# Optimization experiments

Measured on AMD Instinct MI355X. Metric: run time of the kernel, lower is better.

The kernel has to match this reference:

```python
import jax, jax.numpy as jnp
import numpy as np

B, S, D = 2, 1024, 768
NH = 12
DH = D // NH
HID = 1536
G, EPG = 4, 2
E = G * EPG
TEMP = 1.0
LN_EPS = 1e-5


def setup_inputs() -> dict:
    key = jax.random.key(0)
    ks = jax.random.split(key, 8)
    s = 0.02
    return {
        "x": jax.random.normal(ks[0], (B, S, D), jnp.float32),
        "ln1_w": jnp.ones((D,), jnp.float32),
        "ln1_b": jnp.zeros((D,), jnp.float32),
        "in_proj_w": jax.random.normal(ks[1], (3 * D, D), jnp.float32) * s,
        "in_proj_b": jnp.zeros((3 * D,), jnp.float32),
        "out_proj_w": jax.random.normal(ks[2], (D, D), jnp.float32) * s,
        "out_proj_b": jnp.zeros((D,), jnp.float32),
        "ln2_w": jnp.ones((D,), jnp.float32),
        "ln2_b": jnp.zeros((D,), jnp.float32),
        "Wg": jax.random.normal(ks[3], (D, G), jnp.float32) * s,
        "bg": jnp.zeros((G,), jnp.float32),
        "We": jax.random.normal(ks[4], (G, D, EPG), jnp.float32) * s,
        "be": jnp.zeros((G, EPG), jnp.float32),
        "W1": jax.random.normal(ks[5], (E, D, HID), jnp.float32) * s,
        "b1": jnp.zeros((E, HID), jnp.float32),
        "W2": jax.random.normal(ks[6], (E, HID, D), jnp.float32) * s,
        "b2": jnp.zeros((E, D), jnp.float32),
    }


def _ln(x, w, b):
    m = x.mean(-1, keepdims=True)
    v = x.var(-1, keepdims=True)
    return (x - m) / jnp.sqrt(v + LN_EPS) * w + b


def _mha(h, wqkv, bqkv, wo, bo):
    qkv = h @ wqkv.T + bqkv                       # [B,S,3D]
    q, k, v = jnp.split(qkv, 3, axis=-1)
    q = q.reshape(B, S, NH, DH)
    k = k.reshape(B, S, NH, DH)
    v = v.reshape(B, S, NH, DH)
    scale = 1.0 / np.sqrt(DH).astype(np.float32)
    att = jnp.einsum("bqhd,bkhd->bhqk", q, k) * scale
    p = jax.nn.softmax(att, axis=-1)
    o = jnp.einsum("bhqk,bkhd->bqhd", p, v).reshape(B, S, D)
    return o @ wo.T + bo


def _moe(h, Wg, bg, We, be, W1, b1, W2, b2):
    hf = h.reshape(-1, D)                         # [N,D] tokens
    # level-1: group router (temperature softmax, top-1)
    gp = jax.nn.softmax((hf @ Wg + bg) / TEMP, axis=-1)          # [N,G]
    g = jnp.argmax(gp, axis=-1)                                   # [N]
    pg = jnp.take_along_axis(gp, g[:, None], axis=1)[:, 0]        # [N]
    # level-2: within-group expert router
    el = jnp.einsum("nd,gde->nge", hf, We) + be                   # [N,G,EPG]
    ep = jax.nn.softmax(el / TEMP, axis=-1)
    ep_g = jnp.take_along_axis(ep, g[:, None, None], axis=1)[:, 0, :]  # [N,EPG]
    e = jnp.argmax(ep_g, axis=-1)                                 # [N]
    pe = jnp.take_along_axis(ep_g, e[:, None], axis=1)[:, 0]      # [N]
    flat = g * EPG + e                                            # flat expert id [N]
    combine = jax.nn.one_hot(flat, E, dtype=hf.dtype) * (pg * pe)[:, None]  # [N,E]
    # dense expert compute (reference form of dispatch/grouped-GEMM/combine)
    hid = jax.nn.gelu(jnp.einsum("nd,edh->enh", hf, W1) + b1[:, None, :])   # [E,N,HID]
    y = jnp.einsum("enh,ehd->end", hid, W2) + b2[:, None, :]                # [E,N,D]
    out = jnp.einsum("ne,end->nd", combine, y)                              # [N,D]
    return out.reshape(h.shape)


def reference(x, ln1_w, ln1_b, in_proj_w, in_proj_b, out_proj_w, out_proj_b,
              ln2_w, ln2_b, Wg, bg, We, be, W1, b1, W2, b2):
    a = _mha(_ln(x, ln1_w, ln1_b), in_proj_w, in_proj_b, out_proj_w, out_proj_b)
    x = x + a  # dropout p=0.0 -> identity
    m = _moe(_ln(x, ln2_w, ln2_b), Wg, bg, We, be, W1, b1, W2, b2)
    return x + m
```

## Files before the change

### kernel.cpp

```cpp
#include <hip/hip_runtime.h>
#include <stdint.h>

#define B_ 2
#define S_ 1024
#define D_ 768
#define NH_ 12
#define DH_ 64
#define HID_ 1536
#define G_ 4
#define EPG_ 2
#define E_ 8
#define NTOK (B_*S_)
#define NGRP (B_*NH_*16)
#define KSPLIT 3

typedef unsigned short u16;
typedef unsigned int u32;
typedef __bf16 bf16x8 __attribute__((ext_vector_type(8)));
typedef float f32x4 __attribute__((ext_vector_type(4)));
typedef u16 u16x4 __attribute__((ext_vector_type(4)));
typedef u16 u16x8 __attribute__((ext_vector_type(8)));
typedef u32 u32x4 __attribute__((ext_vector_type(4)));

struct BfPair { u16 hi, lo; };

__device__ __forceinline__ u16 f2bf(float f){
  unsigned u = __builtin_bit_cast(unsigned, f);
  u += 0x7FFFu + ((u >> 16) & 1u);
  return (u16)(u >> 16);
}
__device__ __forceinline__ float bf2f(u16 h){
  unsigned u = ((unsigned)h) << 16;
  return __builtin_bit_cast(float, u);
}
__device__ __forceinline__ BfPair split_bf(float v){
  BfPair p;
  p.hi = f2bf(v);
  p.lo = f2bf(v - bf2f(p.hi));
  return p;
}
__device__ __forceinline__ float gelu_tanh(float x){
  float t = 0.7978845608028654f * (x + 0.044715f * x * x * x);
  float e = __expf(2.f * t);
  float th = 1.f - 2.f / (e + 1.f);
  return 0.5f * x * (1.f + th);
}
__device__ __forceinline__ void gload_lds16(const void* g, void* l){
  __builtin_amdgcn_global_load_lds(
      (const __attribute__((address_space(1))) void*)g,
      (__attribute__((address_space(3))) void*)l, 16, 0, 0);
}

__global__ __launch_bounds__(256) void k_prep(
    const float* __restrict__ in_proj_w, const float* __restrict__ out_proj_w,
    const float* __restrict__ W1, const float* __restrict__ W2,
    u16* __restrict__ inpTh, u16* __restrict__ inpTl,
    u16* __restrict__ outpTh, u16* __restrict__ outpTl,
    u16* __restrict__ W1t, u16* __restrict__ W2t){
  __shared__ float tile[32][33];
  int bid = blockIdx.x, t = threadIdx.x;
  if (bid < 2304){
    const float* src; u16 *dh, *dl; int i;
    if (bid < 1728){ src = in_proj_w; dh = inpTh; dl = inpTl; i = bid * 256 + t; }
    else           { src = out_proj_w; dh = outpTh; dl = outpTl; i = (bid - 1728) * 256 + t; }
    float4 v = ((const float4*)src)[i];
    u16x4 oh, ol;
    BfPair p0 = split_bf(v.x), p1 = split_bf(v.y), p2 = split_bf(v.z), p3 = split_bf(v.w);
    oh.x = p0.hi; ol.x = p0.lo; oh.y = p1.hi; ol.y = p1.lo;
    oh.z = p2.hi; ol.z = p2.lo; oh.w = p3.hi; ol.w = p3.lo;
    ((u16x4*)dh)[i] = oh;
    ((u16x4*)dl)[i] = ol;
  } else {
    const float* src; u16* dst; int R, C, cx, cy, e;
    if (bid < 11520){
      int r = bid - 2304; e = r / 1152; r %= 1152;
      R = D_; C = HID_; cx = r % 48; cy = r / 48;
      src = W1; dst = W1t;
    } else {
      int r = bid - 11520; e = r / 1152; r %= 1152;
      R = HID_; C = D_; cx = r % 24; cy = r / 24;
      src = W2; dst = W2t;
    }
    const float* s = src + (size_t)e * R * C;
    u16* d = dst + (size_t)e * R * C;
    int c0 = cx * 32, r0 = cy * 32;
    int tx = t & 31, ty = t >> 5;
    #pragma unroll
    for (int i = 0; i < 32; i += 8)
      tile[ty + i][tx] = s[(size_t)(r0 + ty + i) * C + c0 + tx];
    __syncthreads();
    #pragma unroll
    for (int i = 0; i < 32; i += 8)
      d[(size_t)(c0 + ty + i) * R + r0 + tx] = f2bf(tile[tx][ty + i]);
  }
}

__global__ __launch_bounds__(256) void k_layernorm(
    const float* __restrict__ x, const float* __restrict__ w, const float* __restrict__ b,
    u16* __restrict__ oh, u16* __restrict__ ol, float* __restrict__ of){
  int row = blockIdx.x;
  const float* xr = x + (size_t)row * D_;
  int t = threadIdx.x;
  float v0 = xr[t], v1 = xr[t + 256], v2 = xr[t + 512];
  float s = v0 + v1 + v2;
  float sq = v0 * v0 + v1 * v1 + v2 * v2;
  #pragma unroll
  for (int m = 1; m < 64; m <<= 1){ s += __shfl_xor(s, m); sq += __shfl_xor(sq, m); }
  __shared__ float ls[4], lq[4];
  int wid = t >> 6;
  if ((t & 63) == 0){ ls[wid] = s; lq[wid] = sq; }
  __syncthreads();
  s = ls[0] + ls[1] + ls[2] + ls[3];
  sq = lq[0] + lq[1] + lq[2] + lq[3];
  float mean = s * (1.f / D_);
  float var = sq * (1.f / D_) - mean * mean;
  float rstd = rsqrtf(var + 1e-5f);
  #pragma unroll
  for (int i = 0; i < 3; i++){
    int dcol = t + i * 256;
    float v = (i == 0 ? v0 : (i == 1 ? v1 : v2));
    float y = (v - mean) * rstd * w[dcol] + b[dcol];
    BfPair p = split_bf(y);
    oh[(size_t)row * D_ + dcol] = p.hi;
    if (ol) ol[(size_t)row * D_ + dcol] = p.lo;
    if (of) of[(size_t)row * D_ + dcol] = y;
  }
}

template<int EPI>
__global__ __launch_bounds__(256) void k_gemm3(
    const u16* __restrict__ Ah, const u16* __restrict__ Al,
    const u16* __restrict__ Bh, const u16* __restrict__ Bl,
    const float* __restrict__ bias, const float* __restrict__ resid,
    u16* __restrict__ outh, u16* __restrict__ outl, float* __restrict__ outf,
    u16* __restrict__ vth, u16* __restrict__ vtl,
    int M, int N, int K){
  __shared__ alignas(16) u16 Ash[2][128 * 32];
  __shared__ alignas(16) u16 Asl[2][128 * 32];
  __shared__ alignas(16) u16 Bsh[2][64 * 32];
  __shared__ alignas(16) u16 Bsl[2][64 * 32];
  int m0 = blockIdx.x * 128, n0 = blockIdx.y * 64;
  int tid = threadIdx.x, w = tid >> 6, l = tid & 63;
  f32x4 acc[2][4];
  #pragma unroll
  for (int i = 0; i < 2; i++)
    #pragma unroll
    for (int j = 0; j < 4; j++) acc[i][j] = f32x4{0.f, 0.f, 0.f, 0.f};
  int srow = l >> 2;
  int scol = 8 * ((l & 3) ^ ((l >> 2) & 3));
  const u16* gAh0 = Ah + (size_t)(m0 + w * 32 + srow) * K + scol;
  const u16* gAh1 = gAh0 + (size_t)16 * K;
  const u16* gAl0 = Al + (size_t)(m0 + w * 32 + srow) * K + scol;
  const u16* gAl1 = gAl0 + (size_t)16 * K;
  const u16* gBh = Bh + (size_t)(n0 + w * 16 + srow) * K + scol;
  const u16* gBl = Bl + (size_t)(n0 + w * 16 + srow) * K + scol;
  int dA0 = (w * 32) * 32, dA1 = (w * 32 + 16) * 32, dB = (w * 16) * 32;
  auto STAGE = [&](int buf, int k0){
    gload_lds16(gAh0 + k0, &Ash[buf][dA0]);
    gload_lds16(gAh1 + k0, &Ash[buf][dA1]);
    gload_lds16(gAl0 + k0, &Asl[buf][dA0]);
    gload_lds16(gAl1 + k0, &Asl[buf][dA1]);
    gload_lds16(gBh + k0, &Bsh[buf][dB]);
    gload_lds16(gBl + k0, &Bsl[buf][dB]);
  };
  STAGE(0, 0);
  __syncthreads();
  int nk = K / 32;
  int ca = (l >> 4) ^ (l & 3);
  int ai0 = (w * 32 + (l & 15)) * 32 + 8 * ca;
  int ai1 = ai0 + 16 * 32;
  for (int t = 0; t < nk; t++){
    int cur = t & 1;
    if (t + 1 < nk) STAGE(cur ^ 1, (t + 1) * 32);
    bf16x8 afh[2], afl[2], bfh[4], bfl[4];
    afh[0] = *(const bf16x8*)&Ash[cur][ai0];
    afh[1] = *(const bf16x8*)&Ash[cur][ai1];
    afl[0] = *(const bf16x8*)&Asl[cur][ai0];
    afl[1] = *(const bf16x8*)&Asl[cur][ai1];
    #pragma unroll
    for (int ni = 0; ni < 4; ni++){
      int bi = (ni * 16 + (l & 15)) * 32 + 8 * ca;
      bfh[ni] = *(const bf16x8*)&Bsh[cur][bi];
      bfl[ni] = *(const bf16x8*)&Bsl[cur][bi];
    }
    #pragma unroll
    for (int mi = 0; mi < 2; mi++)
      #pragma unroll
      for (int ni = 0; ni < 4; ni++){
        acc[mi][ni] = __builtin_amdgcn_mfma_f32_16x16x32_bf16(afh[mi], bfh[ni], acc[mi][ni], 0, 0, 0);
        acc[mi][ni] = __builtin_amdgcn_mfma_f32_16x16x32_bf16(afh[mi], bfl[ni], acc[mi][ni], 0, 0, 0);
        acc[mi][ni] = __builtin_amdgcn_mfma_f32_16x16x32_bf16(afl[mi], bfh[ni], acc[mi][ni], 0, 0, 0);
      }
    __syncthreads();
  }
  int r4 = (l >> 4) * 4, cc = l & 15;
  if (EPI == 0 && n0 >= 2 * D_){
    int hh = (n0 - 2 * D_) >> 6;
    int bb = m0 / S_;
    int bhl = bb * NH_ + hh;
    int sg0 = m0 % S_;
    u16* VhL = (u16*)&Ash[0][0];
    u16* VlL = (u16*)&Asl[0][0];
    #pragma unroll
    for (int mi = 0; mi < 2; mi++){
      #pragma unroll
      for (int ni = 0; ni < 4; ni++){
        int d = ni * 16 + cc;
        float bv = bias ? bias[n0 + d] : 0.f;
        int sl = w * 32 + mi * 16 + r4;
        u16x4 h4, l4;
        #pragma unroll
        for (int r = 0; r < 4; r++){
          BfPair p = split_bf(acc[mi][ni][r] + bv);
          h4[r] = p.hi; l4[r] = p.lo;
        }
        *(u16x4*)&VhL[d * 128 + sl] = h4;
        *(u16x4*)&VlL[d * 128 + sl] = l4;
      }
    }
    __syncthreads();
    for (int i = tid; i < 64 * 16; i += 256){
      int d = i >> 4, s8 = (i & 15) * 8;
      size_t go = ((size_t)bhl * DH_ + d) * S_ + sg0 + s8;
      *(u16x8*)&vth[go] = *(const u16x8*)&VhL[d * 128 + s8];
      *(u16x8*)&vtl[go] = *(const u16x8*)&VlL[d * 128 + s8];
    }
    return;
  }
  #pragma unroll
  for (int mi = 0; mi < 2; mi++){
    #pragma unroll
    for (int ni = 0; ni < 4; ni++){
      int col = n0 + ni * 16 + cc;
      float bv = bias ? bias[col] : 0.f;
      #pragma unroll
      for (int r = 0; r < 4; r++){
        int row = m0 + w * 32 + mi * 16 + r4 + r;
        float v = acc[mi][ni][r] + bv;
        if (EPI == 0){
          BfPair p = split_bf(v);
          outh[(size_t)row * N + col] = p.hi;
          outl[(size_t)row * N + col] = p.lo;
        } else {
          outf[(size_t)row * N + col] = v + resid[(size_t)row * N + col];
        }
      }
    }
  }
}

__global__ __launch_bounds__(256) void k_attn3(
    const u16* __restrict__ qkvh, const u16* __restrict__ qkvl,
    const u16* __restrict__ vth, const u16* __restrict__ vtl,
    float* __restrict__ po0, float* __restrict__ po1, float* __restrict__ po2,
    float* __restrict__ pm, float* __restrict__ plsum){
  __shared__ alignas(16) u16 Ksh[2][32 * 64];
  __shared__ alignas(16) u16 Ksl[2][32 * 64];
  __shared__ alignas(16) u16 Vsh[2][64 * 32];
  __shared__ alignas(16) u16 Vsl[2][64 * 32];
  int bh = blockIdx.x, qb = blockIdx.y, ks = blockIdx.z;
  int b = bh / NH_, h = bh % NH_;
  int g = bh * 16 + qb;
  int tid = threadIdx.x, w = tid >> 6, l = tid & 63;
  int q0 = qb * 64 + w * 16;
  const int RS = 3 * D_;
  size_t qoff = (size_t)(b * S_ + q0 + (l & 15)) * RS + h * DH_ + 8 * (l >> 4);
  bf16x8 aqh[2], aql[2];
  aqh[0] = *(const bf16x8*)(qkvh + qoff); aqh[1] = *(const bf16x8*)(qkvh + qoff + 32);
  aql[0] = *(const bf16x8*)(qkvl + qoff); aql[1] = *(const bf16x8*)(qkvl + qoff + 32);
  f32x4 oacc[4];
  #pragma unroll
  for (int i = 0; i < 4; i++) oacc[i] = f32x4{0.f, 0.f, 0.f, 0.f};
  float mrun = -1e30f, lrun = 0.f;

  size_t koff = (size_t)(b * S_ + w * 8 + (l >> 3)) * RS + D_ + h * DH_ + 8 * ((l & 7) ^ (l >> 3));
  const u16* Kgh = qkvh + koff;
  const u16* Kgl = qkvl + koff;
  size_t voff = ((size_t)bh * DH_ + w * 16 + (l >> 2)) * S_ + 8 * ((l & 3) ^ ((l >> 2) & 3));
  const u16* Vgh = vth + voff;
  const u16* Vgl = vtl + voff;
  int wdst = w * 512;

  auto STAGE = [&](int buf, int akt){
    gload_lds16(Kgh + (size_t)(akt * 32) * RS, &Ksh[buf][wdst]);
    gload_lds16(Kgl + (size_t)(akt * 32) * RS, &Ksl[buf][wdst]);
    gload_lds16(Vgh + akt * 32, &Vsh[buf][wdst]);
    gload_lds16(Vgl + akt * 32, &Vsl[buf][wdst]);
  };
  int kt0 = (ks * 32) / KSPLIT;
  int ktE = ((ks + 1) * 32) / KSPLIT;
  STAGE(0, kt0);
  __syncthreads();

  int ck0 = (l >> 4) ^ (l & 7);
  int ck1 = ck0 ^ 4;
  int cv = (l >> 4) ^ (l & 3);
  int s1 = (l & 15) | ((l & 16) << 1);
  int s2 = s1 + 16;
  bool up = (l & 32) != 0;

  for (int kt = kt0; kt < ktE; kt++){
    int cur = (kt - kt0) & 1;
    if (kt + 1 < ktE) STAGE(cur ^ 1, kt + 1);
    f32x4 st[2];
    #pragma unroll
    for (int nt = 0; nt < 2; nt++){
      int rbase = (nt * 16 + (l & 15)) * 64;
      bf16x8 kh0 = *(const bf16x8*)&Ksh[cur][rbase + 8 * ck0];
      bf16x8 kh1 = *(const bf16x8*)&Ksh[cur][rbase + 8 * ck1];
      bf16x8 kl0 = *(const bf16x8*)&Ksl[cur][rbase + 8 * ck0];
      bf16x8 kl1 = *(const bf16x8*)&Ksl[cur][rbase + 8 * ck1];
      f32x4 c = f32x4{0.f, 0.f, 0.f, 0.f};
      c = __builtin_amdgcn_mfma_f32_16x16x32_bf16(kh0, aqh[0], c, 0, 0, 0);
      c = __builtin_amdgcn_mfma_f32_16x16x32_bf16(kh1, aqh[1], c, 0, 0, 0);
      c = __builtin_amdgcn_mfma_f32_16x16x32_bf16(kh0, aql[0], c, 0, 0, 0);
      c = __builtin_amdgcn_mfma_f32_16x16x32_bf16(kh1, aql[1], c, 0, 0, 0);
      c = __builtin_amdgcn_mfma_f32_16x16x32_bf16(kl0, aqh[0], c, 0, 0, 0);
      c = __builtin_amdgcn_mfma_f32_16x16x32_bf16(kl1, aqh[1], c, 0, 0, 0);
      st[nt] = c;
    }
    float mx = fmaxf(fmaxf(fmaxf(st[0][0], st[0][1]), fmaxf(st[0][2], st[0][3])),
                     fmaxf(fmaxf(st[1][0], st[1][1]), fmaxf(st[1][2], st[1][3])));
    mx = fmaxf(mx, __shfl_xor(mx, 16));
    mx = fmaxf(mx, __shfl_xor(mx, 32));
    mx *= 0.125f;
    if (!__all(mx <= mrun)){
      float mnew = fmaxf(mrun, mx);
      float alpha = __expf(mrun - mnew);
      lrun *= alpha;
      #pragma unroll
      for (int r = 0; r < 4; r++){
        float ar = __shfl(alpha, (l & 48) | (((l >> 4) << 2) + r));
        oacc[0][r] *= ar; oacc[1][r] *= ar; oacc[2][r] *= ar; oacc[3][r] *= ar;
      }
      mrun = mnew;
    }
    float p[8]; float sum = 0.f;
    #pragma unroll
    for (int j = 0; j < 8; j++){
      p[j] = __expf(st[j >> 2][j & 3] * 0.125f - mrun);
      sum += p[j];
    }
    sum += __shfl_xor(sum, 16);
    sum += __shfl_xor(sum, 32);
    lrun += sum;
    u32 pkh[4], pkl[4];
    #pragma unroll
    for (int i = 0; i < 4; i++){
      BfPair a = split_bf(p[2 * i]), bb = split_bf(p[2 * i + 1]);
      pkh[i] = (u32)a.hi | ((u32)bb.hi << 16);
      pkl[i] = (u32)a.lo | ((u32)bb.lo << 16);
    }
    u32 ah0 = __shfl((int)pkh[0], s1), ah1 = __shfl((int)pkh[1], s1);
    u32 ah2 = __shfl((int)pkh[2], s1), ah3 = __shfl((int)pkh[3], s1);
    u32 bh0 = __shfl((int)pkh[0], s2), bh1 = __shfl((int)pkh[1], s2);
    u32 bh2 = __shfl((int)pkh[2], s2), bh3 = __shfl((int)pkh[3], s2);
    u32 al0 = __shfl((int)pkl[0], s1), al1 = __shfl((int)pkl[1], s1);
    u32 al2 = __shfl((int)pkl[2], s1), al3 = __shfl((int)pkl[3], s1);
    u32 bl0 = __shfl((int)pkl[0], s2), bl1 = __shfl((int)pkl[1], s2);
    u32 bl2 = __shfl((int)pkl[2], s2), bl3 = __shfl((int)pkl[3], s2);
    u32x4 fh, fl;
    fh.x = up ? ah2 : ah0; fh.y = up ? ah3 : ah1; fh.z = up ? bh2 : bh0; fh.w = up ? bh3 : bh1;
    fl.x = up ? al2 : al0; fl.y = up ? al3 : al1; fl.z = up ? bl2 : bl0; fl.w = up ? bl3 : bl1;
    bf16x8 pa_h = __builtin_bit_cast(bf16x8, fh);
    bf16x8 pa_l = __builtin_bit_cast(bf16x8, fl);
    #pragma unroll
    for (int dt = 0; dt < 4; dt++){
      int vb = (dt * 16 + (l & 15)) * 32 + 8 * cv;
      bf16x8 bvh = *(const bf16x8*)&Vsh[cur][vb];
      bf16x8 bvl = *(const bf16x8*)&Vsl[cur][vb];
      oacc[dt] = __builtin_amdgcn_mfma_f32_16x16x32_bf16(pa_h, bvh, oacc[dt], 0, 0, 0);
      oacc[dt] = __builtin_amdgcn_mfma_f32_16x16x32_bf16(pa_h, bvl, oacc[dt], 0, 0, 0);
      oacc[dt] = __builtin_amdgcn_mfma_f32_16x16x32_bf16(pa_l, bvh, oacc[dt], 0, 0, 0);
    }
    __syncthreads();
  }
  float* po = (ks == 0) ? po0 : ((ks == 1) ? po1 : po2);
  #pragma unroll
  for (int dt = 0; dt < 4; dt++)
    #pragma unroll
    for (int r = 0; r < 4; r++){
      int qloc = w * 16 + (l >> 4) * 4 + r;
      int d = dt * 16 + (l & 15);
      po[((size_t)(g * 64 + qloc)) * 64 + d] = oacc[dt][r];
    }
  if (l < 16){
    pm[(ks * NGRP + g) * 64 + w * 16 + l] = mrun;
    plsum[(ks * NGRP + g) * 64 + w * 16 + l] = lrun;
  }
}

__global__ __launch_bounds__(256) void k_attn_merge(
    const float* __restrict__ po0, const float* __restrict__ po1, const float* __restrict__ po2,
    const float* __restrict__ pm, const float* __restrict__ plsum,
    u16* __restrict__ oh, u16* __restrict__ ol){
  int bh = blockIdx.x, qb = blockIdx.y;
  int b = bh / NH_, h = bh % NH_;
  int g = bh * 16 + qb;
  int t = threadIdx.x;
  int q = t >> 2, d0 = (t & 3) * 16;
  float m0 = pm[g * 64 + q];
  float m1 = pm[(NGRP + g) * 64 + q];
  float m2 = pm[(2 * NGRP + g) * 64 + q];
  float l0 = plsum[g * 64 + q];
  float l1 = plsum[(NGRP + g) * 64 + q];
  float l2 = plsum[(2 * NGRP + g) * 64 + q];
  float M = fmaxf(fmaxf(m0, m1), m2);
  float a0 = __expf(m0 - M), a1 = __expf(m1 - M), a2 = __expf(m2 - M);
  float rcp = 1.f / (l0 * a0 + l1 * a1 + l2 * a2);
  size_t base = ((size_t)(g * 64 + q)) * 64 + d0;
  size_t orow = (size_t)(b * S_ + qb * 64 + q) * D_ + h * DH_ + d0;
  #pragma unroll
  for (int j = 0; j < 16; j++){
    float v = (po0[base + j] * a0 + po1[base + j] * a1 + po2[base + j] * a2) * rcp;
    BfPair p = split_bf(v);
    oh[orow + j] = p.hi;
    ol[orow + j] = p.lo;
  }
}

__global__ __launch_bounds__(256) void k_router(
    const float* __restrict__ h2f, const float* __restrict__ Wg, const float* __restrict__ bg,
    const float* __restrict__ We, const float* __restrict__ be,
    int* __restrict__ flat, float* __restrict__ pc){
  int w = threadIdx.x >> 6, l = threadIdx.x & 63;
  int n = blockIdx.x * 4 + w;
  const float* hr = h2f + (size_t)n * D_;
  float pl[4] = {0.f, 0.f, 0.f, 0.f};
  for (int d = l; d < D_; d += 64){
    float hv = hr[d];
    float4 wg = *(const float4*)&Wg[d * 4];
    pl[0] += hv * wg.x; pl[1] += hv * wg.y; pl[2] += hv * wg.z; pl[3] += hv * wg.w;
  }
  #pragma unroll
  for (int m = 1; m < 64; m <<= 1)
    #pragma unroll
    for (int g = 0; g < 4; g++) pl[g] += __shfl_xor(pl[g], m);
  float lg[4];
  #pragma unroll
  for (int g = 0; g < 4; g++) lg[g] = pl[g] + bg[g];
  int gi = 0; float gm = lg[0];
  #pragma unroll
  for (int g = 1; g < 4; g++) if (lg[g] > gm){ gm = lg[g]; gi = g; }
  float gs = 0.f;
  #pragma unroll
  for (int g = 0; g < 4; g++) gs += expf(lg[g] - gm);
  float pg = 1.f / gs;
  float e0 = 0.f, e1 = 0.f;
  for (int d = l; d < D_; d += 64){
    float hv = hr[d];
    float2 we = *(const float2*)&We[((size_t)gi * D_ + d) * 2];
    e0 += hv * we.x; e1 += hv * we.y;
  }
  #pragma unroll
  for (int m = 1; m < 64; m <<= 1){ e0 += __shfl_xor(e0, m); e1 += __shfl_xor(e1, m); }
  e0 += be[gi * 2]; e1 += be[gi * 2 + 1];
  int ei; float pe;
  if (e1 > e0){ ei = 1; pe = 1.f / (1.f + expf(e0 - e1)); }
  else        { ei = 0; pe = 1.f / (1.f + expf(e1 - e0)); }
  if (l == 0){
    flat[n] = gi * 2 + ei;
    pc[n] = pg * pe;
  }
}

__global__ __launch_bounds__(1024) void k_bucket(
    const int* __restrict__ flat, int* __restrict__ moeI, int* __restrict__ order){
  __shared__ int cnt[E_], off[E_], cur[E_];
  int t = threadIdx.x;
  if (t < E_){ cnt[t] = 0; cur[t] = 0; }
  __syncthreads();
  int n0 = t, n1 = t + 1024;
  int f0 = flat[n0], f1 = flat[n1];
  atomicAdd(&cnt[f0], 1);
  atomicAdd(&cnt[f1], 1);
  __syncthreads();
  if (t == 0){
    int s = 0;
    for (int e = 0; e < E_; e++){
      off[e] = s; moeI[16 + e] = s; moeI[e] = cnt[e]; s += cnt[e];
    }
  }
  __syncthreads();
  int p0 = atomicAdd(&cur[f0], 1);
  order[off[f0] + p0] = n0;
  int p1 = atomicAdd(&cur[f1], 1);
  order[off[f1] + p1] = n1;
}

__global__ __launch_bounds__(256) void k_moe_gemm1(
    const u16* __restrict__ h2, const u16* __restrict__ W1t, const float* __restrict__ b1,
    const int* __restrict__ order, const int* __restrict__ moeI, u16* __restrict__ hid){
  int e = blockIdx.x, mt = blockIdx.y, nt = blockIdx.z;
  int cnt = moeI[e];
  if (mt * 64 >= cnt) return;
  int off = moeI[16 + e];
  __shared__ alignas(16) u16 As[2][64 * 64];
  __shared__ alignas(16) u16 Bs[2][64 * 64];
  int tid = threadIdx.x, w = tid >> 6, l = tid & 63;
  int wr = w >> 1, wc = w & 1;
  f32x4 acc[2][2];
  #pragma unroll
  for (int i = 0; i < 2; i++)
    #pragma unroll
    for (int j = 0; j < 2; j++) acc[i][j] = f32x4{0.f, 0.f, 0.f, 0.f};
  int r0 = w * 16 + (l >> 3);
  int sch = 8 * ((l & 7) ^ (l >> 3));
  int tokA0 = order[off + min(mt * 64 + r0, cnt - 1)];
  int tokA1 = order[off + min(mt * 64 + r0 + 8, cnt - 1)];
  const u16* gA0 = h2 + (size_t)tokA0 * D_ + sch;
  const u16* gA1 = h2 + (size_t)tokA1 * D_ + sch;
  const u16* gB0 = W1t + (size_t)e * HID_ * D_ + (size_t)(nt * 64 + r0) * D_ + sch;
  const u16* gB1 = gB0 + (size_t)8 * D_;
  int d0 = (w * 16) * 64, d1 = (w * 16 + 8) * 64;
  auto STAGE = [&](int buf, int k0){
    gload_lds16(gA0 + k0, &As[buf][d0]);
    gload_lds16(gA1 + k0, &As[buf][d1]);
    gload_lds16(gB0 + k0, &Bs[buf][d0]);
    gload_lds16(gB1 + k0, &Bs[buf][d1]);
  };
  STAGE(0, 0);
  __syncthreads();
  int c0 = (l >> 4) ^ (l & 7);
  int c1 = ((l >> 4) + 4) ^ (l & 7);
  const int nk = D_ / 64;
  for (int t = 0; t < nk; t++){
    int cur = t & 1;
    if (t + 1 < nk) STAGE(cur ^ 1, (t + 1) * 64);
    bf16x8 af[2][2], bfr[2][2];
    #pragma unroll
    for (int mi = 0; mi < 2; mi++){
      int rbase = (wr * 32 + mi * 16 + (l & 15)) * 64;
      af[mi][0] = *(const bf16x8*)&As[cur][rbase + 8 * c0];
      af[mi][1] = *(const bf16x8*)&As[cur][rbase + 8 * c1];
    }
    #pragma unroll
    for (int ni = 0; ni < 2; ni++){
      int rbase = (wc * 32 + ni * 16 + (l & 15)) * 64;
      bfr[ni][0] = *(const bf16x8*)&Bs[cur][rbase + 8 * c0];
      bfr[ni][1] = *(const bf16x8*)&Bs[cur][rbase + 8 * c1];
    }
    #pragma unroll
    for (int mi = 0; mi < 2; mi++)
      #pragma unroll
      for (int ni = 0; ni < 2; ni++){
        acc[mi][ni] = __builtin_amdgcn_mfma_f32_16x16x32_bf16(af[mi][0], bfr[ni][0], acc[mi][ni], 0, 0, 0);
        acc[mi][ni] = __builtin_amdgcn_mfma_f32_16x16x32_bf16(af[mi][1], bfr[ni][1], acc[mi][ni], 0, 0, 0);
      }
    __syncthreads();
  }
  int r4 = (l >> 4) * 4, cc = l & 15;
  #pragma unroll
  for (int mi = 0; mi < 2; mi++){
    #pragma unroll
    for (int ni = 0; ni < 2; ni++){
      int col = nt * 64 + wc * 32 + ni * 16 + cc;
      float bv = b1[e * HID_ + col];
      #pragma unroll
      for (int r = 0; r < 4; r++){
        int rowl = mt * 64 + wr * 32 + mi * 16 + r4 + r;
        if (rowl < cnt){
          float v = gelu_tanh(acc[mi][ni][r] + bv);
          hid[(size_t)(off + rowl) * HID_ + col] = f2bf(v);
        }
      }
    }
  }
}

__global__ __launch_bounds__(256) void k_moe_gemm2(
    const u16* __restrict__ hid, const u16* __restrict__ W2t, const float* __restrict__ b2,
    const int* __restrict__ order, const int* __restrict__ moeI,
    const float* __restrict__ pc, const float* __restrict__ x2, float* __restrict__ out){
  int e = blockIdx.x, mt = blockIdx.y, nt = blockIdx.z;
  int cnt = moeI[e];
  if (mt * 64 >= cnt) return;
  int off = moeI[16 + e];
  __shared__ alignas(16) u16 As[2][64 * 64];
  __shared__ alignas(16) u16 Bs[2][64 * 64];
  int tid = threadIdx.x, w = tid >> 6, l = tid & 63;
  int wr = w >> 1, wc = w & 1;
  f32x4 acc[2][2];
  #pragma unroll
  for (int i = 0; i < 2; i++)
    #pragma unroll
    for (int j = 0; j < 2; j++) acc[i][j] = f32x4{0.f, 0.f, 0.f, 0.f};
  int r0 = w * 16 + (l >> 3);
  int sch = 8 * ((l & 7) ^ (l >> 3));
  int ar0 = off + min(mt * 64 + r0, cnt - 1);
  int ar1 = off + min(mt * 64 + r0 + 8, cnt - 1);
  const u16* gA0 = hid + (size_t)ar0 * HID_ + sch;
  const u16* gA1 = hid + (size_t)ar1 * HID_ + sch;
  const u16* gB0 = W2t + (size_t)e * D_ * HID_ + (size_t)(nt * 64 + r0) * HID_ + sch;
  const u16* gB1 = gB0 + (size_t)8 * HID_;
  int d0 = (w * 16) * 64, d1 = (w * 16 + 8) * 64;
  auto STAGE = [&](int buf, int k0){
    gload_lds16(gA0 + k0, &As[buf][d0]);
    gload_lds16(gA1 + k0, &As[buf][d1]);
    gload_lds16(gB0 + k0, &Bs[buf][d0]);
    gload_lds16(gB1 + k0, &Bs[buf][d1]);
  };
  STAGE(0, 0);
  __syncthreads();
  int c0 = (l >> 4) ^ (l & 7);
  int c1 = ((l >> 4) + 4) ^ (l & 7);
  const int nk = HID_ / 64;
  for (int t = 0; t < nk; t++){
    int cur = t & 1;
    if (t + 1 < nk) STAGE(cur ^ 1, (t + 1) * 64);
    bf16x8 af[2][2], bfr[2][2];
    #pragma unroll
    for (int mi = 0; mi < 2; mi++){
      int rbase = (wr * 32 + mi * 16 + (l & 15)) * 64;
      af[mi][0] = *(const bf16x8*)&As[cur][rbase + 8 * c0];
      af[mi][1] = *(const bf16x8*)&As[cur][rbase + 8 * c1];
    }
    #pragma unroll
    for (int ni = 0; ni < 2; ni++){
      int rbase = (wc * 32 + ni * 16 + (l & 15)) * 64;
      bfr[ni][0] = *(const bf16x8*)&Bs[cur][rbase + 8 * c0];
      bfr[ni][1] = *(const bf16x8*)&Bs[cur][rbase + 8 * c1];
    }
    #pragma unroll
    for (int mi = 0; mi < 2; mi++)
      #pragma unroll
      for (int ni = 0; ni < 2; ni++){
        acc[mi][ni] = __builtin_amdgcn_mfma_f32_16x16x32_bf16(af[mi][0], bfr[ni][0], acc[mi][ni], 0, 0, 0);
        acc[mi][ni] = __builtin_amdgcn_mfma_f32_16x16x32_bf16(af[mi][1], bfr[ni][1], acc[mi][ni], 0, 0, 0);
      }
    __syncthreads();
  }
  int r4 = (l >> 4) * 4, cc = l & 15;
  #pragma unroll
  for (int mi = 0; mi < 2; mi++){
    #pragma unroll
    for (int r = 0; r < 4; r++){
      int rowl = mt * 64 + wr * 32 + mi * 16 + r4 + r;
      if (rowl < cnt){
        int tok = order[off + rowl];
        float pv = pc[tok];
        #pragma unroll
        for (int ni = 0; ni < 2; ni++){
          int col = nt * 64 + wc * 32 + ni * 16 + cc;
          float v = acc[mi][ni][r] + b2[e * D_ + col];
          out[(size_t)tok * D_ + col] = x2[(size_t)tok * D_ + col] + pv * v;
        }
      }
    }
  }
}

extern "C" void kernel_launch(void* const* d_in, const int* in_sizes, int n_in,
                              void* d_out, int out_size, void* d_ws, size_t ws_size,
                              hipStream_t stream){
  const float* x         = (const float*)d_in[0];
  const float* ln1_w     = (const float*)d_in[1];
  const float* ln1_b     = (const float*)d_in[2];
  const float* in_proj_w = (const float*)d_in[3];
  const float* in_proj_b = (const float*)d_in[4];
  const float* out_proj_w= (const float*)d_in[5];
  const float* out_proj_b= (const float*)d_in[6];
  const float* ln2_w     = (const float*)d_in[7];
  const float* ln2_b     = (const float*)d_in[8];
  const float* Wg        = (const float*)d_in[9];
  const float* bg        = (const float*)d_in[10];
  const float* We        = (const float*)d_in[11];
  const float* be        = (const float*)d_in[12];
  const float* W1        = (const float*)d_in[13];
  const float* b1        = (const float*)d_in[14];
  const float* W2        = (const float*)d_in[15];
  const float* b2        = (const float*)d_in[16];
  float* out = (float*)d_out;

  char* ws = (char*)d_ws;
  size_t off = 0;
  auto alloc = [&](size_t bytes) -> char* {
    char* p = ws + off;
    off += (bytes + 255) & ~(size_t)255;
    return p;
  };
  u16*   inpTh = (u16*)  alloc((size_t)3 * D_ * D_ * 2);
  u16*   inpTl = (u16*)  alloc((size_t)3 * D_ * D_ * 2);
  u16*   outpTh= (u16*)  alloc((size_t)D_ * D_ * 2);
  u16*   outpTl= (u16*)  alloc((size_t)D_ * D_ * 2);
  u16*   W1t  = (u16*)  alloc((size_t)E_ * HID_ * D_ * 2);
  u16*   W2t  = (u16*)  alloc((size_t)E_ * D_ * HID_ * 2);
  u16*   qkvh = (u16*)  alloc((size_t)NTOK * 3 * D_ * 2);
  u16*   qkvl = (u16*)  alloc((size_t)NTOK * 3 * D_ * 2);
  u16*   h1h  = (u16*)  alloc((size_t)NTOK * D_ * 2);
  u16*   h1l  = (u16*)  alloc((size_t)NTOK * D_ * 2);
  u16*   vth  = (u16*)  alloc((size_t)B_ * NH_ * DH_ * S_ * 2);
  u16*   vtl  = (u16*)  alloc((size_t)B_ * NH_ * DH_ * S_ * 2);
  float* x2   = (float*)alloc((size_t)NTOK * D_ * 4);
  u16*   h2   = (u16*)  alloc((size_t)NTOK * D_ * 2);
  int*   flat = (int*)  alloc(NTOK * 4);
  float* pc   = (float*)alloc(NTOK * 4);
  int*   order= (int*)  alloc(NTOK * 4);
  int*   moeI = (int*)  alloc(32 * 4);
  float* po0  = (float*)h1h;
  float* po1  = (float*)inpTh;
  float* po2  = x2;
  float* pmArr= (float*)((char*)inpTh + 6291456);
  float* plArr= (float*)((char*)inpTh + 6291456 + 294912);
  u16*   attnh= qkvh;
  u16*   attnl= qkvl;
  float* h2f  = (float*)qkvh;
  u16*   hid  = (u16*)qkvl;

  k_prep<<<dim3(20736), dim3(256), 0, stream>>>(
      in_proj_w, out_proj_w, W1, W2, inpTh, inpTl, outpTh, outpTl, W1t, W2t);
  k_layernorm<<<dim3(NTOK), dim3(256), 0, stream>>>(x, ln1_w, ln1_b, h1h, h1l, (float*)nullptr);
  k_gemm3<0><<<dim3(NTOK / 128, 3 * D_ / 64), dim3(256), 0, stream>>>(
      h1h, h1l, inpTh, inpTl, in_proj_b, nullptr, qkvh, qkvl, nullptr, vth, vtl, NTOK, 3 * D_, D_);
  k_attn3<<<dim3(B_ * NH_, S_ / 64, KSPLIT), dim3(256), 0, stream>>>(
      qkvh, qkvl, vth, vtl, po0, po1, po2, pmArr, plArr);
  k_attn_merge<<<dim3(B_ * NH_, S_ / 64), dim3(256), 0, stream>>>(
      po0, po1, po2, pmArr, plArr, attnh, attnl);
  k_gemm3<1><<<dim3(NTOK / 128, D_ / 64), dim3(256), 0, stream>>>(
      attnh, attnl, outpTh, outpTl, out_proj_b, x, nullptr, nullptr, x2,
      (u16*)nullptr, (u16*)nullptr, NTOK, D_, D_);
  k_layernorm<<<dim3(NTOK), dim3(256), 0, stream>>>(x2, ln2_w, ln2_b, h2, (u16*)nullptr, h2f);
  k_router<<<dim3(NTOK / 4), dim3(256), 0, stream>>>(h2f, Wg, bg, We, be, flat, pc);
  k_bucket<<<dim3(1), dim3(1024), 0, stream>>>(flat, moeI, order);
  k_moe_gemm1<<<dim3(E_, NTOK / 64, HID_ / 64), dim3(256), 0, stream>>>(h2, W1t, b1, order, moeI, hid);
  k_moe_gemm2<<<dim3(E_, NTOK / 64, D_ / 64), dim3(256), 0, stream>>>(hid, W2t, b2, order, moeI, pc, x2, out);
}
```

Before: 207.7 us.

## Process two 16-row query tiles per wave in split-K attention

Each wave of the attention kernel now handles 32 query rows (two 16-row groups) instead of 16, so each workgroup covers 128 queries and the grid's query dimension halves. Every K/V tile staged into LDS is reused across twice as many queries, which halves the global-to-LDS traffic and the barrier count per query. In exchange, each thread holds more registers (two sets of accumulators, Q fragments and softmax state), which may lower occupancy. The grid also shrinks to 24x8x3 blocks, which may leave compute units underused. Output indexing is rewritten so the merge kernel's layout stays the same.

```diff
diff --git a/kernel.cpp b/kernel.cpp
--- a/kernel.cpp
+++ b/kernel.cpp
@@ -260,18 +260,21 @@
   __shared__ alignas(16) u16 Vsl[2][64 * 32];
   int bh = blockIdx.x, qb = blockIdx.y, ks = blockIdx.z;
   int b = bh / NH_, h = bh % NH_;
-  int g = bh * 16 + qb;
   int tid = threadIdx.x, w = tid >> 6, l = tid & 63;
-  int q0 = qb * 64 + w * 16;
   const int RS = 3 * D_;
-  size_t qoff = (size_t)(b * S_ + q0 + (l & 15)) * RS + h * DH_ + 8 * (l >> 4);
-  bf16x8 aqh[2], aql[2];
-  aqh[0] = *(const bf16x8*)(qkvh + qoff); aqh[1] = *(const bf16x8*)(qkvh + qoff + 32);
-  aql[0] = *(const bf16x8*)(qkvl + qoff); aql[1] = *(const bf16x8*)(qkvl + qoff + 32);
-  f32x4 oacc[4];
-  #pragma unroll
-  for (int i = 0; i < 4; i++) oacc[i] = f32x4{0.f, 0.f, 0.f, 0.f};
-  float mrun = -1e30f, lrun = 0.f;
+  bf16x8 aqh[2][2], aql[2][2];
+  #pragma unroll
+  for (int G = 0; G < 2; G++){
+    size_t qoff = (size_t)(b * S_ + qb * 128 + w * 32 + G * 16 + (l & 15)) * RS + h * DH_ + 8 * (l >> 4);
+    aqh[G][0] = *(const bf16x8*)(qkvh + qoff); aqh[G][1] = *(const bf16x8*)(qkvh + qoff + 32);
+    aql[G][0] = *(const bf16x8*)(qkvl + qoff); aql[G][1] = *(const bf16x8*)(qkvl + qoff + 32);
+  }
+  f32x4 oacc[2][4];
+  #pragma unroll
+  for (int G = 0; G < 2; G++)
+    #pragma unroll
+    for (int i = 0; i < 4; i++) oacc[G][i] = f32x4{0.f, 0.f, 0.f, 0.f};
+  float mrun[2] = {-1e30f, -1e30f}, lrun[2] = {0.f, 0.f};
 
   size_t koff = (size_t)(b * S_ + w * 8 + (l >> 3)) * RS + D_ + h * DH_ + 8 * ((l & 7) ^ (l >> 3));
   const u16* Kgh = qkvh + koff;
@@ -302,7 +305,7 @@
   for (int kt = kt0; kt < ktE; kt++){
     int cur = (kt - kt0) & 1;
     if (kt + 1 < ktE) STAGE(cur ^ 1, kt + 1);
-    f32x4 st[2];
+    f32x4 st[2][2];
     #pragma unroll
     for (int nt = 0; nt < 2; nt++){
       int rbase = (nt * 16 + (l & 15)) * 64;
@@ -310,83 +313,99 @@
       bf16x8 kh1 = *(const bf16x8*)&Ksh[cur][rbase + 8 * ck1];
       bf16x8 kl0 = *(const bf16x8*)&Ksl[cur][rbase + 8 * ck0];
       bf16x8 kl1 = *(const bf16x8*)&Ksl[cur][rbase + 8 * ck1];
-      f32x4 c = f32x4{0.f, 0.f, 0.f, 0.f};
-      c = __builtin_amdgcn_mfma_f32_16x16x32_bf16(kh0, aqh[0], c, 0, 0, 0);
-      c = __builtin_amdgcn_mfma_f32_16x16x32_bf16(kh1, aqh[1], c, 0, 0, 0);
-      c = __builtin_amdgcn_mfma_f32_16x16x32_bf16(kh0, aql[0], c, 0, 0, 0);
-      c = __builtin_amdgcn_mfma_f32_16x16x32_bf16(kh1, aql[1], c, 0, 0, 0);
-      c = __builtin_amdgcn_mfma_f32_16x16x32_bf16(kl0, aqh[0], c, 0, 0, 0);
-      c = __builtin_amdgcn_mfma_f32_16x16x32_bf16(kl1, aqh[1], c, 0, 0, 0);
-      st[nt] = c;
-    }
-    float mx = fmaxf(fmaxf(fmaxf(st[0][0], st[0][1]), fmaxf(st[0][2], st[0][3])),
-                     fmaxf(fmaxf(st[1][0], st[1][1]), fmaxf(st[1][2], st[1][3])));
-    mx = fmaxf(mx, __shfl_xor(mx, 16));
-    mx = fmaxf(mx, __shfl_xor(mx, 32));
-    mx *= 0.125f;
-    if (!__all(mx <= mrun)){
-      float mnew = fmaxf(mrun, mx);
-      float alpha = __expf(mrun - mnew);
-      lrun *= alpha;
-      #pragma unroll
-      for (int r = 0; r < 4; r++){
-        float ar = __shfl(alpha, (l & 48) | (((l >> 4) << 2) + r));
-        oacc[0][r] *= ar; oacc[1][r] *= ar; oacc[2][r] *= ar; oacc[3][r] *= ar;
-      }
-      mrun = mnew;
-    }
-    float p[8]; float sum = 0.f;
-    #pragma unroll
-    for (int j = 0; j < 8; j++){
-      p[j] = __expf(st[j >> 2][j & 3] * 0.125f - mrun);
-      sum += p[j];
-    }
-    sum += __shfl_xor(sum, 16);
-    sum += __shfl_xor(sum, 32);
-    lrun += sum;
-    u32 pkh[4], pkl[4];
-    #pragma unroll
-    for (int i = 0; i < 4; i++){
-      BfPair a = split_bf(p[2 * i]), bb = split_bf(p[2 * i + 1]);
-      pkh[i] = (u32)a.hi | ((u32)bb.hi << 16);
-      pkl[i] = (u32)a.lo | ((u32)bb.lo << 16);
-    }
-    u32 ah0 = __shfl((int)pkh[0], s1), ah1 = __shfl((int)pkh[1], s1);
-    u32 ah2 = __shfl((int)pkh[2], s1), ah3 = __shfl((int)pkh[3], s1);
-    u32 bh0 = __shfl((int)pkh[0], s2), bh1 = __shfl((int)pkh[1], s2);
-    u32 bh2 = __shfl((int)pkh[2], s2), bh3 = __shfl((int)pkh[3], s2);
-    u32 al0 = __shfl((int)pkl[0], s1), al1 = __shfl((int)pkl[1], s1);
-    u32 al2 = __shfl((int)pkl[2], s1), al3 = __shfl((int)pkl[3], s1);
-    u32 bl0 = __shfl((int)pkl[0], s2), bl1 = __shfl((int)pkl[1], s2);
-    u32 bl2 = __shfl((int)pkl[2], s2), bl3 = __shfl((int)pkl[3], s2);
-    u32x4 fh, fl;
-    fh.x = up ? ah2 : ah0; fh.y = up ? ah3 : ah1; fh.z = up ? bh2 : bh0; fh.w = up ? bh3 : bh1;
-    fl.x = up ? al2 : al0; fl.y = up ? al3 : al1; fl.z = up ? bl2 : bl0; fl.w = up ? bl3 : bl1;
-    bf16x8 pa_h = __builtin_bit_cast(bf16x8, fh);
-    bf16x8 pa_l = __builtin_bit_cast(bf16x8, fl);
+      #pragma unroll
+      for (int G = 0; G < 2; G++){
+        f32x4 c = f32x4{0.f, 0.f, 0.f, 0.f};
+        c = __builtin_amdgcn_mfma_f32_16x16x32_bf16(kh0, aqh[G][0], c, 0, 0, 0);
+        c = __builtin_amdgcn_mfma_f32_16x16x32_bf16(kh1, aqh[G][1], c, 0, 0, 0);
+        c = __builtin_amdgcn_mfma_f32_16x16x32_bf16(kh0, aql[G][0], c, 0, 0, 0);
+        c = __builtin_amdgcn_mfma_f32_16x16x32_bf16(kh1, aql[G][1], c, 0, 0, 0);
+        c = __builtin_amdgcn_mfma_f32_16x16x32_bf16(kl0, aqh[G][0], c, 0, 0, 0);
+        c = __builtin_amdgcn_mfma_f32_16x16x32_bf16(kl1, aqh[G][1], c, 0, 0, 0);
+        st[G][nt] = c;
+      }
+    }
+    bf16x8 pah[2], pal[2];
+    #pragma unroll
+    for (int G = 0; G < 2; G++){
+      float mx = fmaxf(fmaxf(fmaxf(st[G][0][0], st[G][0][1]), fmaxf(st[G][0][2], st[G][0][3])),
+                       fmaxf(fmaxf(st[G][1][0], st[G][1][1]), fmaxf(st[G][1][2], st[G][1][3])));
+      mx = fmaxf(mx, __shfl_xor(mx, 16));
+      mx = fmaxf(mx, __shfl_xor(mx, 32));
+      mx *= 0.125f;
+      if (!__all(mx <= mrun[G])){
+        float mnew = fmaxf(mrun[G], mx);
+        float alpha = __expf(mrun[G] - mnew);
+        lrun[G] *= alpha;
+        #pragma unroll
+        for (int r = 0; r < 4; r++){
+          float ar = __shfl(alpha, (l & 48) | (((l >> 4) << 2) + r));
+          oacc[G][0][r] *= ar; oacc[G][1][r] *= ar; oacc[G][2][r] *= ar; oacc[G][3][r] *= ar;
+        }
+        mrun[G] = mnew;
+      }
+      float p[8]; float sum = 0.f;
+      #pragma unroll
+      for (int j = 0; j < 8; j++){
+        p[j] = __expf(st[G][j >> 2][j & 3] * 0.125f - mrun[G]);
+        sum += p[j];
+      }
+      sum += __shfl_xor(sum, 16);
+      sum += __shfl_xor(sum, 32);
+      lrun[G] += sum;
+      u32 pkh[4], pkl[4];
+      #pragma unroll
+      for (int i = 0; i < 4; i++){
+        BfPair a = split_bf(p[2 * i]), bb = split_bf(p[2 * i + 1]);
+        pkh[i] = (u32)a.hi | ((u32)bb.hi << 16);
+        pkl[i] = (u32)a.lo | ((u32)bb.lo << 16);
+      }
+      u32 ah0 = __shfl((int)pkh[0], s1), ah1 = __shfl((int)pkh[1], s1);
+      u32 ah2 = __shfl((int)pkh[2], s1), ah3 = __shfl((int)pkh[3], s1);
+      u32 bh0 = __shfl((int)pkh[0], s2), bh1 = __shfl((int)pkh[1], s2);
+      u32 bh2 = __shfl((int)pkh[2], s2), bh3 = __shfl((int)pkh[3], s2);
+      u32 al0 = __shfl((int)pkl[0], s1), al1 = __shfl((int)pkl[1], s1);
+      u32 al2 = __shfl((int)pkl[2], s1), al3 = __shfl((int)pkl[3], s1);
+      u32 bl0 = __shfl((int)pkl[0], s2), bl1 = __shfl((int)pkl[1], s2);
+      u32 bl2 = __shfl((int)pkl[2], s2), bl3 = __shfl((int)pkl[3], s2);
+      u32x4 fh, fl;
+      fh.x = up ? ah2 : ah0; fh.y = up ? ah3 : ah1; fh.z = up ? bh2 : bh0; fh.w = up ? bh3 : bh1;
+      fl.x = up ? al2 : al0; fl.y = up ? al3 : al1; fl.z = up ? bl2 : bl0; fl.w = up ? bl3 : bl1;
+      pah[G] = __builtin_bit_cast(bf16x8, fh);
+      pal[G] = __builtin_bit_cast(bf16x8, fl);
+    }
     #pragma unroll
     for (int dt = 0; dt < 4; dt++){
       int vb = (dt * 16 + (l & 15)) * 32 + 8 * cv;
       bf16x8 bvh = *(const bf16x8*)&Vsh[cur][vb];
       bf16x8 bvl = *(const bf16x8*)&Vsl[cur][vb];
-      oacc[dt] = __builtin_amdgcn_mfma_f32_16x16x32_bf16(pa_h, bvh, oacc[dt], 0, 0, 0);
-      oacc[dt] = __builtin_amdgcn_mfma_f32_16x16x32_bf16(pa_h, bvl, oacc[dt], 0, 0, 0);
-      oacc[dt] = __builtin_amdgcn_mfma_f32_16x16x32_bf16(pa_l, bvh, oacc[dt], 0, 0, 0);
+      #pragma unroll
+      for (int G = 0; G < 2; G++){
+        oacc[G][dt] = __builtin_amdgcn_mfma_f32_16x16x32_bf16(pah[G], bvh, oacc[G][dt], 0, 0, 0);
+        oacc[G][dt] = __builtin_amdgcn_mfma_f32_16x16x32_bf16(pah[G], bvl, oacc[G][dt], 0, 0, 0);
+        oacc[G][dt] = __builtin_amdgcn_mfma_f32_16x16x32_bf16(pal[G], bvh, oacc[G][dt], 0, 0, 0);
+      }
     }
     __syncthreads();
   }
   float* po = (ks == 0) ? po0 : ((ks == 1) ? po1 : po2);
   #pragma unroll
-  for (int dt = 0; dt < 4; dt++)
-    #pragma unroll
-    for (int r = 0; r < 4; r++){
-      int qloc = w * 16 + (l >> 4) * 4 + r;
-      int d = dt * 16 + (l & 15);
-      po[((size_t)(g * 64 + qloc)) * 64 + d] = oacc[dt][r];
-    }
+  for (int G = 0; G < 2; G++)
+    #pragma unroll
+    for (int dt = 0; dt < 4; dt++)
+      #pragma unroll
+      for (int r = 0; r < 4; r++){
+        int qg = qb * 128 + w * 32 + G * 16 + (l >> 4) * 4 + r;
+        int d = dt * 16 + (l & 15);
+        po[((size_t)(bh * 1024 + qg)) * 64 + d] = oacc[G][dt][r];
+      }
   if (l < 16){
-    pm[(ks * NGRP + g) * 64 + w * 16 + l] = mrun;
-    plsum[(ks * NGRP + g) * 64 + w * 16 + l] = lrun;
+    #pragma unroll
+    for (int G = 0; G < 2; G++){
+      int qg = qb * 128 + w * 32 + G * 16 + l;
+      pm[ks * (NGRP * 64) + bh * 1024 + qg] = mrun[G];
+      plsum[ks * (NGRP * 64) + bh * 1024 + qg] = lrun[G];
+    }
   }
 }
 
@@ -712,7 +731,7 @@
   k_layernorm<<<dim3(NTOK), dim3(256), 0, stream>>>(x, ln1_w, ln1_b, h1h, h1l, (float*)nullptr);
   k_gemm3<0><<<dim3(NTOK / 128, 3 * D_ / 64), dim3(256), 0, stream>>>(
       h1h, h1l, inpTh, inpTl, in_proj_b, nullptr, qkvh, qkvl, nullptr, vth, vtl, NTOK, 3 * D_, D_);
-  k_attn3<<<dim3(B_ * NH_, S_ / 64, KSPLIT), dim3(256), 0, stream>>>(
+  k_attn3<<<dim3(B_ * NH_, S_ / 128, KSPLIT), dim3(256), 0, stream>>>(
       qkvh, qkvl, vth, vtl, po0, po1, po2, pmArr, plArr);
   k_attn_merge<<<dim3(B_ * NH_, S_ / 64), dim3(256), 0, stream>>>(
       po0, po1, po2, pmArr, plArr, attnh, attnl);
```

Result: slower. 217.1 us (+4.5%).
